# Kernel optimization log

Hardware: AMD Instinct MI355X
Metric: run time of the kernel (lower is better)

## Reference

```python
import jax, jax.numpy as jnp
import numpy as np

N, D, C = 1024, 512, 85742
S, M, EPS = 64.0, 0.5, 1e-07  # arcface defaults


def setup_inputs() -> dict:
    key = jax.random.key(0)
    k1, k2, k3 = jax.random.split(key, 3)
    x = jax.random.normal(k1, (N, D), dtype=jnp.float32)
    W = jax.random.normal(k2, (C, D), dtype=jnp.float32) * 0.05
    labels = jax.random.randint(k3, (N,), 0, C, dtype=jnp.int64)
    return {"x": x, "W": W, "labels": labels, "positive": 1}


def reference(x, W, labels, positive):
    # L2-normalize x rows (torch F.normalize semantics, eps=1e-12).
    # NOTE: the original torch code's weight-normalization loop is a no-op,
    # so W is used unnormalized, faithfully reproduced here.
    xn = x / jnp.maximum(jnp.linalg.norm(x, axis=1, keepdims=True), 1e-12)
    wf = xn @ W.T  # [N, C] cosine-like logits (W unnormalized)
    if not positive:
        return wf
    rows = jnp.arange(wf.shape[0])
    target = wf[rows, labels]  # diagonal gather
    # arcface margin: s * cos(acos(clamped) + m)
    numerator = S * jnp.cos(jnp.arccos(jnp.clip(target, -1.0 + EPS, 1.0 - EPS)) + M)
    # masked exp-sum over non-target classes (replaces Python-loop excl)
    exp_all = jnp.exp(S * wf)
    excl_sum = jnp.sum(exp_all, axis=1) - exp_all[rows, labels]
    denominator = jnp.exp(numerator) + excl_sum
    L = numerator - jnp.log(denominator)
    return (wf, -jnp.mean(L))
```

## Files before the change

kernel.cpp:

```cpp
#include <hip/hip_runtime.h>
#include <hip/hip_bf16.h>

#define NROW 1024
#define DDIM 512
#define CDIM 85742
#define SSC 64.0f
#define MARG 0.5f
#define AEPS 1e-7f

typedef __attribute__((ext_vector_type(8))) short bf16x8;
typedef __attribute__((ext_vector_type(4))) float f32x4;

__device__ __forceinline__ void async_ld16(const void* g, void* l) {
  __builtin_amdgcn_global_load_lds((const __attribute__((address_space(1))) void*)g,
                                   (__attribute__((address_space(3))) void*)l, 16, 0, 0);
}

__global__ void row_normalize(const float* __restrict__ x, __hip_bfloat16* __restrict__ xn) {
  const int row = blockIdx.x;
  const int lane = threadIdx.x;
  const float4* xr = (const float4*)(x + (size_t)row * DDIM);
  float4 a = xr[lane * 2 + 0];
  float4 b = xr[lane * 2 + 1];
  float ss = a.x * a.x + a.y * a.y + a.z * a.z + a.w * a.w +
             b.x * b.x + b.y * b.y + b.z * b.z + b.w * b.w;
#pragma unroll
  for (int o = 32; o >= 1; o >>= 1) ss += __shfl_xor(ss, o);
  const float inv = 1.0f / fmaxf(sqrtf(ss), 1e-12f);
  __hip_bfloat16 t[8];
  t[0] = __float2bfloat16(a.x * inv); t[1] = __float2bfloat16(a.y * inv);
  t[2] = __float2bfloat16(a.z * inv); t[3] = __float2bfloat16(a.w * inv);
  t[4] = __float2bfloat16(b.x * inv); t[5] = __float2bfloat16(b.y * inv);
  t[6] = __float2bfloat16(b.z * inv); t[7] = __float2bfloat16(b.w * inv);
  *(bf16x8*)(xn + (size_t)row * DDIM + lane * 8) = *(bf16x8*)t;
}

__global__ void convert_w(const float* __restrict__ W, __hip_bfloat16* __restrict__ Wb) {
  const int n8 = CDIM * DDIM / 8;
  int i = blockIdx.x * blockDim.x + threadIdx.x;
  const int stride = gridDim.x * blockDim.x;
  for (; i < n8; i += stride) {
    float4 a = ((const float4*)W)[(size_t)i * 2 + 0];
    float4 b = ((const float4*)W)[(size_t)i * 2 + 1];
    __hip_bfloat16 t[8];
    t[0] = __float2bfloat16(a.x); t[1] = __float2bfloat16(a.y);
    t[2] = __float2bfloat16(a.z); t[3] = __float2bfloat16(a.w);
    t[4] = __float2bfloat16(b.x); t[5] = __float2bfloat16(b.y);
    t[6] = __float2bfloat16(b.z); t[7] = __float2bfloat16(b.w);
    ((bf16x8*)Wb)[i] = *(bf16x8*)t;
  }
}

template <bool WB16>
__global__ __launch_bounds__(256) void gemm_loss(const __hip_bfloat16* __restrict__ A,
                                                 const void* __restrict__ Wsrc,
                                                 float* __restrict__ wf,
                                                 float* __restrict__ rowsum) {
  __shared__ __hip_bfloat16 As[128 * 32];
  __shared__ __hip_bfloat16 Bs[128 * 32];
  const int tid = threadIdx.x;
  const int lane = tid & 63;
  const int wav = tid >> 6;
  const int wm = wav >> 1, wn = wav & 1;
  const int row0 = blockIdx.x * 128;
  const int col0 = blockIdx.y * 128;
  const int lr = lane & 15, lq = lane >> 4;
  const int ldsWaveBase = (tid & ~63) * 8;

  f32x4 acc[4][4] = {};

  for (int k0 = 0; k0 < DDIM; k0 += 32) {
#pragma unroll
    for (int q = 0; q < 2; ++q) {
      const int chunk = q * 256 + tid;
      const int r = chunk >> 2, kc = chunk & 3;
      async_ld16(A + ((size_t)(row0 + r) * DDIM + k0 + kc * 8),
                 As + (q * 256 * 8 + ldsWaveBase));
    }
    if (WB16) {
      const __hip_bfloat16* Wb = (const __hip_bfloat16*)Wsrc;
#pragma unroll
      for (int q = 0; q < 2; ++q) {
        const int chunk = q * 256 + tid;
        const int r = chunk >> 2, kc = chunk & 3;
        int gr = col0 + r;
        gr = gr < CDIM ? gr : CDIM - 1;
        async_ld16(Wb + ((size_t)gr * DDIM + k0 + kc * 8),
                   Bs + (q * 256 * 8 + ldsWaveBase));
      }
    } else {
      const float* Wf = (const float*)Wsrc;
#pragma unroll
      for (int q = 0; q < 2; ++q) {
        const int chunk = q * 256 + tid;
        const int r = chunk >> 2, kc = chunk & 3;
        int gr = col0 + r;
        gr = gr < CDIM ? gr : CDIM - 1;
        const float4* g = (const float4*)(Wf + (size_t)gr * DDIM + k0 + kc * 8);
        float4 va = g[0], vb = g[1];
        __hip_bfloat16 t[8];
        t[0] = __float2bfloat16(va.x); t[1] = __float2bfloat16(va.y);
        t[2] = __float2bfloat16(va.z); t[3] = __float2bfloat16(va.w);
        t[4] = __float2bfloat16(vb.x); t[5] = __float2bfloat16(vb.y);
        t[6] = __float2bfloat16(vb.z); t[7] = __float2bfloat16(vb.w);
        *(bf16x8*)(Bs + chunk * 8) = *(bf16x8*)t;
      }
    }
    __syncthreads();

    bf16x8 af[4], bfr[4];
#pragma unroll
    for (int i = 0; i < 4; ++i) {
      af[i]  = *(const bf16x8*)(As + (wm * 64 + i * 16 + lr) * 32 + lq * 8);
      bfr[i] = *(const bf16x8*)(Bs + (wn * 64 + i * 16 + lr) * 32 + lq * 8);
    }
#pragma unroll
    for (int i = 0; i < 4; ++i)
#pragma unroll
      for (int j = 0; j < 4; ++j)
        acc[i][j] = __builtin_amdgcn_mfma_f32_16x16x32_bf16(af[i], bfr[j], acc[i][j], 0, 0, 0);
    __syncthreads();
  }

#pragma unroll
  for (int i = 0; i < 4; ++i) {
    const int rb = row0 + wm * 64 + i * 16 + lq * 4;
#pragma unroll
    for (int r = 0; r < 4; ++r) {
      const int grow = rb + r;
      float esum = 0.f;
#pragma unroll
      for (int j = 0; j < 4; ++j) {
        const int gcol = col0 + wn * 64 + j * 16 + lr;
        const float v = acc[i][j][r];
        if (gcol < CDIM) {
          wf[(size_t)grow * CDIM + gcol] = v;
          esum += __expf(SSC * v);
        }
      }
      esum += __shfl_xor(esum, 1);
      esum += __shfl_xor(esum, 2);
      esum += __shfl_xor(esum, 4);
      esum += __shfl_xor(esum, 8);
      if (lr == 0) atomicAdd(rowsum + grow, esum);
    }
  }
}

__global__ void finalize(const float* __restrict__ wf, const float* __restrict__ rowsum,
                         const int* __restrict__ labels, float* __restrict__ out_loss) {
  const int i = threadIdx.x;
  const int lab = labels[i];
  const float tgt = wf[(size_t)i * CDIM + lab];
  const float tc = fminf(fmaxf(tgt, -1.0f + AEPS), 1.0f - AEPS);
  const float num = SSC * cosf(acosf(tc) + MARG);
  const float excl = rowsum[i] - __expf(SSC * tgt);
  float L = num - logf(__expf(num) + excl);
#pragma unroll
  for (int o = 32; o >= 1; o >>= 1) L += __shfl_xor(L, o);
  __shared__ float red[16];
  if ((i & 63) == 0) red[i >> 6] = L;
  __syncthreads();
  if (i < 64) {
    float v = (i < 16) ? red[i] : 0.f;
#pragma unroll
    for (int o = 8; o >= 1; o >>= 1) v += __shfl_xor(v, o);
    if (i == 0) out_loss[0] = -v * (1.0f / NROW);
  }
}

extern "C" void kernel_launch(void* const* d_in, const int* in_sizes, int n_in,
                              void* d_out, int out_size, void* d_ws, size_t ws_size,
                              hipStream_t stream) {
  const float* x = (const float*)d_in[0];
  const float* W = (const float*)d_in[1];
  const int* labels = (const int*)d_in[2];
  float* out = (float*)d_out;

  float* rowsum = (float*)d_ws;
  __hip_bfloat16* xn = (__hip_bfloat16*)((char*)d_ws + 4096);
  __hip_bfloat16* Wb = (__hip_bfloat16*)((char*)d_ws + 4096 + (size_t)NROW * DDIM * 2);
  const size_t need = 4096 + (size_t)NROW * DDIM * 2 + (size_t)CDIM * DDIM * 2;
  const bool wb16 = ws_size >= need;

  hipMemsetAsync(d_ws, 0, 4096, stream);
  row_normalize<<<NROW, 64, 0, stream>>>(x, xn);

  dim3 grid(8, (CDIM + 127) / 128);
  if (wb16) {
    convert_w<<<2048, 256, 0, stream>>>(W, Wb);
    gemm_loss<true><<<grid, 256, 0, stream>>>(xn, (const void*)Wb, out, rowsum);
  } else {
    gemm_loss<false><<<grid, 256, 0, stream>>>(xn, (const void*)W, out, rowsum);
  }
  finalize<<<1, 1024, 0, stream>>>(out, rowsum, labels, out + (size_t)NROW * CDIM);
}
```

Measured before the change: 718.2 us.

## Fuse W bf16 conversion into GEMM via async fp32 LDS loads and XCD-aware tile mapping

Removes the separate convert_w pass and the memset. W is now loaded as fp32 directly into LDS with async global_load_lds using an XOR swizzle, then converted to bf16 in registers before the MFMA. The grid is remapped to a 1D launch in which each XCD owns a contiguous range of column tiles, with the 8 row tiles of a column tile adjacent in launch order so the W tile can be reused from that XCD's L2. The rowsum zeroing moves into row_normalize. This drops one full pass over W (a read plus a bf16 write) in exchange for twice the LDS footprint and bytes for B, plus per-iteration conversion work.

```diff
diff --git a/kernel.cpp b/kernel.cpp
--- a/kernel.cpp
+++ b/kernel.cpp
@@ -16,9 +16,11 @@
                                    (__attribute__((address_space(3))) void*)l, 16, 0, 0);
 }
 
-__global__ void row_normalize(const float* __restrict__ x, __hip_bfloat16* __restrict__ xn) {
+__global__ void row_normalize(const float* __restrict__ x, __hip_bfloat16* __restrict__ xn,
+                              float* __restrict__ rowsum) {
   const int row = blockIdx.x;
   const int lane = threadIdx.x;
+  if (lane == 0) rowsum[row] = 0.0f;
   const float4* xr = (const float4*)(x + (size_t)row * DDIM);
   float4 a = xr[lane * 2 + 0];
   float4 b = xr[lane * 2 + 1];
@@ -35,37 +37,36 @@
   *(bf16x8*)(xn + (size_t)row * DDIM + lane * 8) = *(bf16x8*)t;
 }
 
-__global__ void convert_w(const float* __restrict__ W, __hip_bfloat16* __restrict__ Wb) {
-  const int n8 = CDIM * DDIM / 8;
-  int i = blockIdx.x * blockDim.x + threadIdx.x;
-  const int stride = gridDim.x * blockDim.x;
-  for (; i < n8; i += stride) {
-    float4 a = ((const float4*)W)[(size_t)i * 2 + 0];
-    float4 b = ((const float4*)W)[(size_t)i * 2 + 1];
-    __hip_bfloat16 t[8];
-    t[0] = __float2bfloat16(a.x); t[1] = __float2bfloat16(a.y);
-    t[2] = __float2bfloat16(a.z); t[3] = __float2bfloat16(a.w);
-    t[4] = __float2bfloat16(b.x); t[5] = __float2bfloat16(b.y);
-    t[6] = __float2bfloat16(b.z); t[7] = __float2bfloat16(b.w);
-    ((bf16x8*)Wb)[i] = *(bf16x8*)t;
-  }
+__device__ __forceinline__ bf16x8 cvt8(f32x4 lo, f32x4 hi) {
+  __hip_bfloat16 t[8];
+  t[0] = __float2bfloat16(lo.x); t[1] = __float2bfloat16(lo.y);
+  t[2] = __float2bfloat16(lo.z); t[3] = __float2bfloat16(lo.w);
+  t[4] = __float2bfloat16(hi.x); t[5] = __float2bfloat16(hi.y);
+  t[6] = __float2bfloat16(hi.z); t[7] = __float2bfloat16(hi.w);
+  return *(bf16x8*)t;
 }
 
-template <bool WB16>
 __global__ __launch_bounds__(256) void gemm_loss(const __hip_bfloat16* __restrict__ A,
-                                                 const void* __restrict__ Wsrc,
+                                                 const float* __restrict__ W,
                                                  float* __restrict__ wf,
                                                  float* __restrict__ rowsum) {
+  const int id = blockIdx.x;
+  const int xcd = id & 7;
+  const int s = id >> 3;
+  const int ctile = xcd * 84 + (s >> 3);
+  if (ctile >= 670) return;
+  const int mtile = s & 7;
+
   __shared__ __hip_bfloat16 As[128 * 32];
-  __shared__ __hip_bfloat16 Bs[128 * 32];
+  __shared__ float Bs[128 * 32];
   const int tid = threadIdx.x;
   const int lane = tid & 63;
   const int wav = tid >> 6;
   const int wm = wav >> 1, wn = wav & 1;
-  const int row0 = blockIdx.x * 128;
-  const int col0 = blockIdx.y * 128;
+  const int row0 = mtile * 128;
+  const int col0 = ctile * 128;
   const int lr = lane & 15, lq = lane >> 4;
-  const int ldsWaveBase = (tid & ~63) * 8;
+  const int waveBase = tid & ~63;
 
   f32x4 acc[4][4] = {};
 
@@ -75,44 +76,32 @@
       const int chunk = q * 256 + tid;
       const int r = chunk >> 2, kc = chunk & 3;
       async_ld16(A + ((size_t)(row0 + r) * DDIM + k0 + kc * 8),
-                 As + (q * 256 * 8 + ldsWaveBase));
+                 As + (q * 256 + waveBase) * 8);
     }
-    if (WB16) {
-      const __hip_bfloat16* Wb = (const __hip_bfloat16*)Wsrc;
 #pragma unroll
-      for (int q = 0; q < 2; ++q) {
-        const int chunk = q * 256 + tid;
-        const int r = chunk >> 2, kc = chunk & 3;
-        int gr = col0 + r;
-        gr = gr < CDIM ? gr : CDIM - 1;
-        async_ld16(Wb + ((size_t)gr * DDIM + k0 + kc * 8),
-                   Bs + (q * 256 * 8 + ldsWaveBase));
-      }
-    } else {
-      const float* Wf = (const float*)Wsrc;
-#pragma unroll
-      for (int q = 0; q < 2; ++q) {
-        const int chunk = q * 256 + tid;
-        const int r = chunk >> 2, kc = chunk & 3;
-        int gr = col0 + r;
-        gr = gr < CDIM ? gr : CDIM - 1;
-        const float4* g = (const float4*)(Wf + (size_t)gr * DDIM + k0 + kc * 8);
-        float4 va = g[0], vb = g[1];
-        __hip_bfloat16 t[8];
-        t[0] = __float2bfloat16(va.x); t[1] = __float2bfloat16(va.y);
-        t[2] = __float2bfloat16(va.z); t[3] = __float2bfloat16(va.w);
-        t[4] = __float2bfloat16(vb.x); t[5] = __float2bfloat16(vb.y);
-        t[6] = __float2bfloat16(vb.z); t[7] = __float2bfloat16(vb.w);
-        *(bf16x8*)(Bs + chunk * 8) = *(bf16x8*)t;
-      }
+    for (int q = 0; q < 4; ++q) {
+      const int chunk = q * 256 + tid;
+      const int r = chunk >> 3, kc = chunk & 7;
+      const int kcs = kc ^ (r & 7);
+      int gr = col0 + r;
+      gr = gr < CDIM ? gr : CDIM - 1;
+      async_ld16(W + ((size_t)gr * DDIM + k0 + kcs * 4),
+                 Bs + (q * 256 + waveBase) * 4);
     }
     __syncthreads();
 
     bf16x8 af[4], bfr[4];
 #pragma unroll
-    for (int i = 0; i < 4; ++i) {
-      af[i]  = *(const bf16x8*)(As + (wm * 64 + i * 16 + lr) * 32 + lq * 8);
-      bfr[i] = *(const bf16x8*)(Bs + (wn * 64 + i * 16 + lr) * 32 + lq * 8);
+    for (int i = 0; i < 4; ++i)
+      af[i] = *(const bf16x8*)(As + (wm * 64 + i * 16 + lr) * 32 + lq * 8);
+#pragma unroll
+    for (int j = 0; j < 4; ++j) {
+      const int br = wn * 64 + j * 16 + lr;
+      const int s0 = (2 * lq) ^ (br & 7);
+      const int s1 = (2 * lq + 1) ^ (br & 7);
+      f32x4 lo = *(const f32x4*)(Bs + br * 32 + s0 * 4);
+      f32x4 hi = *(const f32x4*)(Bs + br * 32 + s1 * 4);
+      bfr[j] = cvt8(lo, hi);
     }
 #pragma unroll
     for (int i = 0; i < 4; ++i)
@@ -179,19 +168,8 @@
 
   float* rowsum = (float*)d_ws;
   __hip_bfloat16* xn = (__hip_bfloat16*)((char*)d_ws + 4096);
-  __hip_bfloat16* Wb = (__hip_bfloat16*)((char*)d_ws + 4096 + (size_t)NROW * DDIM * 2);
-  const size_t need = 4096 + (size_t)NROW * DDIM * 2 + (size_t)CDIM * DDIM * 2;
-  const bool wb16 = ws_size >= need;
 
-  hipMemsetAsync(d_ws, 0, 4096, stream);
-  row_normalize<<<NROW, 64, 0, stream>>>(x, xn);
-
-  dim3 grid(8, (CDIM + 127) / 128);
-  if (wb16) {
-    convert_w<<<2048, 256, 0, stream>>>(W, Wb);
-    gemm_loss<true><<<grid, 256, 0, stream>>>(xn, (const void*)Wb, out, rowsum);
-  } else {
-    gemm_loss<false><<<grid, 256, 0, stream>>>(xn, (const void*)W, out, rowsum);
-  }
+  row_normalize<<<NROW, 64, 0, stream>>>(x, xn, rowsum);
+  gemm_loss<<<672 * 8, 256, 0, stream>>>(xn, W, out, rowsum);
   finalize<<<1, 1024, 0, stream>>>(out, rowsum, labels, out + (size_t)NROW * CDIM);
 }
```

Result: faster. 653.9 us (-8.9%).
